# Optimization experiments

Hardware: AMD Instinct MI355X
Metric: run time of the kernel (lower is better)

The kernel has to match this reference:

```python
import jax, jax.numpy as jnp
import numpy as np

B, NORM_NC, LABEL_NC, STYLE_SIZE, NHIDDEN, H, W, KS = 8, 256, 19, 512, 128, 128, 128, 3
EPS = 1e-5


def conv2d(x, w, b):
    # NCHW conv, stride 1, SAME padding (pw = ks//2)
    y = jax.lax.conv_general_dilated(x, w, window_strides=(1, 1), padding='SAME',
                                     dimension_numbers=('NCHW', 'OIHW', 'NCHW'))
    return y + b[None, :, None, None]


def setup_inputs() -> dict:
    key = jax.random.key(0)
    ks = jax.random.split(key, 16)
    s = 0.05
    return {
        'x': jax.random.normal(ks[0], (B, NORM_NC, H, W), jnp.float32),
        'segmap': jax.random.uniform(ks[1], (B, LABEL_NC, H, W), jnp.float32),
        'style': jax.random.normal(ks[2], (B, LABEL_NC, STYLE_SIZE), jnp.float32),
        'w_shared': jax.random.normal(ks[3], (NHIDDEN, LABEL_NC, KS, KS), jnp.float32) * s,
        'b_shared': jnp.zeros((NHIDDEN,), jnp.float32),
        'w_gamma': jax.random.normal(ks[4], (NORM_NC, NHIDDEN, KS, KS), jnp.float32) * s,
        'b_gamma': jnp.zeros((NORM_NC,), jnp.float32),
        'w_beta': jax.random.normal(ks[5], (NORM_NC, NHIDDEN, KS, KS), jnp.float32) * s,
        'b_beta': jnp.zeros((NORM_NC,), jnp.float32),
        'w_sgamma': jax.random.normal(ks[6], (NORM_NC, STYLE_SIZE, KS, KS), jnp.float32) * s,
        'b_sgamma': jnp.zeros((NORM_NC,), jnp.float32),
        'w_sbeta': jax.random.normal(ks[7], (NORM_NC, STYLE_SIZE, KS, KS), jnp.float32) * s,
        'b_sbeta': jnp.zeros((NORM_NC,), jnp.float32),
        'alpha_beta': jax.random.uniform(ks[8], (1,), jnp.float32),
        'alpha_gamma': jax.random.uniform(ks[9], (1,), jnp.float32),
    }


def reference(x, segmap, style, w_shared, b_shared, w_gamma, b_gamma, w_beta, b_beta,
              w_sgamma, b_sgamma, w_sbeta, b_sbeta, alpha_beta, alpha_gamma):
    # InstanceNorm2d (affine=False): per-(b,c) normalization over HxW, biased var
    mean = jnp.mean(x, axis=(2, 3), keepdims=True)
    var = jnp.var(x, axis=(2, 3), keepdims=True)
    normalized = (x - mean) * jax.lax.rsqrt(var + EPS)

    # segmap already at fm_size == out_size -> nearest interpolate is identity
    actv = jax.nn.relu(conv2d(segmap, w_shared, b_shared))  # (B, nhidden, H, W)

    # fused per-pixel contraction over label channels:
    # (style[b,l,s] * segmap[b,l,h,w]).sum(l) -> (B, style_size, H, W)
    style_map = jnp.einsum('bls,blhw->bshw', style, segmap)

    gamma = conv2d(actv, w_gamma, b_gamma)
    beta = conv2d(actv, w_beta, b_beta)
    gamma_style = conv2d(style_map, w_sgamma, b_sgamma)
    beta_style = conv2d(style_map, w_sbeta, b_sbeta)

    wb = jax.nn.sigmoid(alpha_beta)[0]
    wg = jax.nn.sigmoid(alpha_gamma)[0]
    combined_offset = wb * beta_style + (1.0 - wb) * beta
    combined_scale = wg * gamma_style + (1.0 - wg) * gamma + 1.0
    return normalized * combined_scale + combined_offset
```

## Files before the change

### kernel.cpp

```cpp
#include <hip/hip_runtime.h>
#include <hip/hip_bf16.h>
#include <cstdint>

#define B_ 8
#define LABEL_NC 19
#define H_ 128
#define W_ 128
#define UC 640
#define EPS_ 1e-5f

typedef __attribute__((ext_vector_type(8))) short s8v;
typedef __attribute__((ext_vector_type(4))) float f4v;
typedef __attribute__((ext_vector_type(4))) int i4v;
typedef unsigned short ushort_t;

__device__ __forceinline__ ushort_t f2b(float f) {
    union { float f; uint32_t u; } a; a.f = f;
    uint32_t u = a.u;
    return (ushort_t)((u + 0x7FFFu + ((u >> 16) & 1u)) >> 16);
}

__device__ __forceinline__ void gl2lds16(const ushort_t* g, ushort_t* l) {
    __builtin_amdgcn_global_load_lds(
        (const __attribute__((address_space(1))) unsigned int*)g,
        (__attribute__((address_space(3))) unsigned int*)l, 16, 0, 0);
}

__global__ void __launch_bounds__(256) k_prep(
    const float* __restrict__ w_gamma, const float* __restrict__ w_beta,
    const float* __restrict__ w_sgamma, const float* __restrict__ w_sbeta,
    const float* __restrict__ b_gamma, const float* __restrict__ b_beta,
    const float* __restrict__ b_sgamma, const float* __restrict__ b_sbeta,
    const float* __restrict__ alpha_beta, const float* __restrict__ alpha_gamma,
    ushort_t* __restrict__ Wt, float* __restrict__ bias_s, float* __restrict__ bias_o,
    float* __restrict__ zpage)
{
    float wb = 1.f / (1.f + __expf(-alpha_beta[0]));
    float wg = 1.f / (1.f + __expf(-alpha_gamma[0]));
    int gid = blockIdx.x * 256 + threadIdx.x;
    if (gid < 256) bias_s[gid] = wg * b_sgamma[gid] + (1.f - wg) * b_gamma[gid];
    else if (gid < 512) bias_o[gid - 256] = wb * b_sbeta[gid - 256] + (1.f - wb) * b_beta[gid - 256];
    if (gid < 8192) zpage[gid] = 0.f;

    const int total = 9 * 512 * 640;
    for (int idx = gid; idx < total; idx += gridDim.x * 256) {
        int tap = idx / (512 * 640);
        int r = idx - tap * (512 * 640);
        int co = r / 640, ci = r - co * 640;
        int kh = tap / 3, kw = tap - kh * 3;
        float v;
        if (co < 256) {
            if (ci < 128) v = (1.f - wg) * w_gamma[((co * 128 + ci) * 3 + kh) * 3 + kw];
            else          v = wg * w_sgamma[((co * 512 + (ci - 128)) * 3 + kh) * 3 + kw];
        } else {
            int c2 = co - 256;
            if (ci < 128) v = (1.f - wb) * w_beta[((c2 * 128 + ci) * 3 + kh) * 3 + kw];
            else          v = wb * w_sbeta[((c2 * 512 + (ci - 128)) * 3 + kh) * 3 + kw];
        }
        Wt[idx] = f2b(v);
    }
}

__global__ void __launch_bounds__(256) k_stats(const float* __restrict__ x,
                                               float* __restrict__ mean, float* __restrict__ rstd)
{
    int bc = blockIdx.x;
    const float4* p = (const float4*)(x + (size_t)bc * (H_ * W_));
    float s = 0.f, s2 = 0.f;
    for (int i = threadIdx.x; i < H_ * W_ / 4; i += 256) {
        float4 v = p[i];
        s += v.x + v.y + v.z + v.w;
        s2 += v.x * v.x + v.y * v.y + v.z * v.z + v.w * v.w;
    }
    #pragma unroll
    for (int o = 32; o > 0; o >>= 1) { s += __shfl_xor(s, o); s2 += __shfl_xor(s2, o); }
    __shared__ float red[8];
    int wave = threadIdx.x >> 6, lane = threadIdx.x & 63;
    if (lane == 0) { red[wave] = s; red[wave + 4] = s2; }
    __syncthreads();
    if (threadIdx.x == 0) {
        float ts = red[0] + red[1] + red[2] + red[3];
        float t2 = red[4] + red[5] + red[6] + red[7];
        float m = ts * (1.f / 16384.f);
        float v = t2 * (1.f / 16384.f) - m * m;
        mean[bc] = m;
        rstd[bc] = rsqrtf(v + EPS_);
    }
}

__global__ void __launch_bounds__(256) k_buildU(
    const float* __restrict__ segmap, const float* __restrict__ style,
    const float* __restrict__ w_shared, const float* __restrict__ b_shared,
    ushort_t* __restrict__ U)
{
    int bh = blockIdx.x;
    int b = bh >> 7, h = bh & 127;
    __shared__ float seg[3][LABEL_NC][W_];
    const float* segb = segmap + (size_t)b * (LABEL_NC * H_ * W_);
    for (int idx = threadIdx.x; idx < 3 * LABEL_NC * W_; idx += 256) {
        int w = idx & 127;
        int l = (idx >> 7) % LABEL_NC;
        int rr = idx / (LABEL_NC * W_);
        int hh = h + rr - 1;
        seg[rr][l][w] = (hh >= 0 && hh < H_) ? segb[((size_t)l * H_ + hh) * W_ + w] : 0.f;
    }
    __syncthreads();

    int t = threadIdx.x;
    int w = t & 127;
    int grp = __builtin_amdgcn_readfirstlane(t >> 7);
    ushort_t* Urow = U + (((size_t)(b * H_ + h)) * W_ + w) * UC;

    for (int cb = 0; cb < 4; ++cb) {
        int co0 = grp * 64 + cb * 16;
        float acc[16];
        #pragma unroll
        for (int i = 0; i < 16; ++i) acc[i] = b_shared[co0 + i];
        for (int l = 0; l < LABEL_NC; ++l) {
            #pragma unroll
            for (int kh = 0; kh < 3; ++kh) {
                float sm = (w > 0)   ? seg[kh][l][w - 1] : 0.f;
                float s0 = seg[kh][l][w];
                float sp = (w < 127) ? seg[kh][l][w + 1] : 0.f;
                const float* wp = w_shared + ((size_t)co0 * LABEL_NC + l) * 9 + kh * 3;
                #pragma unroll
                for (int i = 0; i < 16; ++i) {
                    const float* wpi = wp + i * (LABEL_NC * 9);
                    acc[i] += sm * wpi[0] + s0 * wpi[1] + sp * wpi[2];
                }
            }
        }
        #pragma unroll
        for (int i = 0; i < 16; ++i)
            Urow[co0 + i] = f2b(acc[i] > 0.f ? acc[i] : 0.f);
    }

    float segr[LABEL_NC];
    #pragma unroll
    for (int l = 0; l < LABEL_NC; ++l) segr[l] = seg[1][l][w];
    const float* styb = style + (size_t)b * (LABEL_NC * 512);
    for (int sb = 0; sb < 16; ++sb) {
        int s0 = grp * 256 + sb * 16;
        float acc[16];
        #pragma unroll
        for (int i = 0; i < 16; ++i) acc[i] = 0.f;
        for (int l = 0; l < LABEL_NC; ++l) {
            const float* sp = styb + l * 512 + s0;
            float sl = segr[l];
            #pragma unroll
            for (int i = 0; i < 16; ++i) acc[i] += sl * sp[i];
        }
        #pragma unroll
        for (int i = 0; i < 16; ++i) Urow[128 + s0 + i] = f2b(acc[i]);
    }
}

#define BK 32

__global__ void __launch_bounds__(512, 1) k_conv(
    const ushort_t* __restrict__ U, const ushort_t* __restrict__ Wt,
    const ushort_t* __restrict__ zp,
    const float* __restrict__ x, const float* __restrict__ mean, const float* __restrict__ rstd,
    const float* __restrict__ bias_s, const float* __restrict__ bias_o,
    float* __restrict__ out)
{
    int orig = blockIdx.x;
    int wg = (orig & 7) * 128 + (orig >> 3);
    int mtile = wg >> 1;
    int cohalf = wg & 1;
    int b = mtile >> 6;
    int h0 = (mtile & 63) << 1;

    extern __shared__ ushort_t smem[];

    int t = threadIdx.x;
    int wv = t >> 6, ln = t & 63;
    int wm = wv >> 1, wn = wv & 1;

    const ushort_t* Ub = U + (size_t)b * (H_ * W_ * UC);

    f4v acc[4][8] = {};

    auto stage_A = [&](int ci0, int ab) {
        ushort_t* sAb = smem + ab * 16384;
        #pragma unroll
        for (int i = 0; i < 4; ++i) {
            int issue = wv * 4 + i;
            int hh = h0 - 1 + (issue >> 3);
            int w = issue * 16 + (ln >> 2);
            int sl = (ln & 3) ^ ((w >> 1) & 3);
            const ushort_t* src = (hh >= 0 && hh < H_)
                ? Ub + ((size_t)hh * W_ + (w & 127)) * UC + ci0 + (sl << 3)
                : zp + (size_t)ln * 8;
            gl2lds16(src, sAb + (size_t)issue * 512);
        }
    };
    auto stage_B = [&](int tapX, int ci0X, int bi) {
        ushort_t* base = smem + 32768 + bi * 8192;
        #pragma unroll
        for (int j = 0; j < 2; ++j) {
            int issue = wv * 2 + j;
            int c = issue * 16 + (ln >> 2);
            int sl = (ln & 3) ^ ((c >> 1) & 3);
            int gq = (c >> 6) & 1;
            int cbase = ((c >> 7) << 6) + (c & 63);
            int co = gq * 256 + cohalf * 128 + cbase;
            const ushort_t* src = Wt + ((size_t)tapX * 512 + co) * UC + ci0X + (sl << 3);
            gl2lds16(src, base + (size_t)issue * 512);
        }
    };

    stage_A(0, 0);
    stage_B(0, 0, 0);
    stage_B(1, 0, 1);

    for (int ch = 0; ch < 20; ++ch) {
        int ci0 = ch * BK;
        ushort_t* sAb = smem + (ch & 1) * 16384;
        bool lastch = (ch == 19);
        #pragma unroll
        for (int tap = 0; tap < 9; ++tap) {
            const int dhp1 = tap / 3;
            const int dw = tap - dhp1 * 3 - 1;
            const int bi = tap % 3;
            const int bi2 = (tap + 2) % 3;

            if (tap == 8) {
                if (lastch) { asm volatile("s_waitcnt vmcnt(0)" ::: "memory"); }
                else        { asm volatile("s_waitcnt vmcnt(6)" ::: "memory"); }
            } else          { asm volatile("s_waitcnt vmcnt(2)" ::: "memory"); }
            __builtin_amdgcn_s_barrier();

            if (tap < 7)        stage_B(tap + 2, ci0, bi2);
            else if (!lastch) {
                if (tap == 7) { stage_B(0, ci0 + BK, bi2); stage_A(ci0 + BK, (ch + 1) & 1); }
                else          stage_B(1, ci0 + BK, bi2);
            }

            ushort_t* sBb = smem + 32768 + bi * 8192;
            int sd = ln >> 4;
            s8v af[4];
            #pragma unroll
            for (int mi = 0; mi < 4; ++mi) {
                int p = wm * 64 + mi * 16 + (ln & 15);
                int q = (p & 127) + dw;
                int qc = q < 0 ? 0 : (q > 127 ? 127 : q);
                int r = (p >> 7) + dhp1;
                s8v v = *(const s8v*)&sAb[(size_t)(((r * 128 + qc) << 2) + (sd ^ ((qc >> 1) & 3))) * 8];
                if (dw != 0 && (q < 0 || q > 127)) { s8v z = {}; v = z; }
                af[mi] = v;
            }
            s8v bf[8];
            #pragma unroll
            for (int ni = 0; ni < 8; ++ni) {
                int c = wn * 128 + (ni >> 2) * 64 + (ni & 3) * 16 + (ln & 15);
                bf[ni] = *(const s8v*)&sBb[(size_t)((c << 2) + (sd ^ ((c >> 1) & 3))) * 8];
            }
            __builtin_amdgcn_s_setprio(1);
            #pragma unroll
            for (int mi = 0; mi < 4; ++mi)
                #pragma unroll
                for (int ni = 0; ni < 8; ++ni)
                    acc[mi][ni] = __builtin_amdgcn_mfma_f32_16x16x32_bf16(
                        af[mi], bf[ni], acc[mi][ni], 0, 0, 0);
            __builtin_amdgcn_s_setprio(0);
        }
    }

    int bc_base = b * 256;
    #pragma unroll
    for (int ni = 0; ni < 4; ++ni) {
        int chn = cohalf * 128 + wn * 64 + ni * 16 + (ln & 15);
        float bs = bias_s[chn] + 1.f;
        float bo = bias_o[chn];
        float mu = mean[bc_base + chn];
        float rs = rstd[bc_base + chn];
        #pragma unroll
        for (int mi = 0; mi < 4; ++mi) {
            #pragma unroll
            for (int r = 0; r < 4; ++r) {
                int p = wm * 64 + mi * 16 + ((ln >> 4) << 2) + r;
                int hh = h0 + (p >> 7);
                int ww = p & 127;
                size_t xi = (((size_t)(bc_base + chn)) * H_ + hh) * W_ + ww;
                float xn = (x[xi] - mu) * rs;
                out[xi] = xn * (acc[mi][ni][r] + bs) + (acc[mi][ni + 4][r] + bo);
            }
        }
    }
}

extern "C" void kernel_launch(void* const* d_in, const int* in_sizes, int n_in,
                              void* d_out, int out_size, void* d_ws, size_t ws_size,
                              hipStream_t stream)
{
    const float* x        = (const float*)d_in[0];
    const float* segmap   = (const float*)d_in[1];
    const float* style    = (const float*)d_in[2];
    const float* w_shared = (const float*)d_in[3];
    const float* b_shared = (const float*)d_in[4];
    const float* w_gamma  = (const float*)d_in[5];
    const float* b_gamma  = (const float*)d_in[6];
    const float* w_beta   = (const float*)d_in[7];
    const float* b_beta   = (const float*)d_in[8];
    const float* w_sgamma = (const float*)d_in[9];
    const float* b_sgamma = (const float*)d_in[10];
    const float* w_sbeta  = (const float*)d_in[11];
    const float* b_sbeta  = (const float*)d_in[12];
    const float* alpha_beta  = (const float*)d_in[13];
    const float* alpha_gamma = (const float*)d_in[14];
    float* out = (float*)d_out;

    char* ws = (char*)d_ws;
    float*    ws_mean  = (float*)(ws + 0);
    float*    ws_rstd  = (float*)(ws + 8192);
    float*    ws_bs    = (float*)(ws + 16384);
    float*    ws_bo    = (float*)(ws + 18432);
    ushort_t* ws_Wt    = (ushort_t*)(ws + 20480);
    ushort_t* ws_zp    = (ushort_t*)(ws + 6 * 1024 * 1024 - 65536);
    ushort_t* ws_U     = (ushort_t*)(ws + 6 * 1024 * 1024);

    (void)hipFuncSetAttribute((const void*)k_conv,
                              hipFuncAttributeMaxDynamicSharedMemorySize, 114688);

    k_prep<<<dim3(2048), dim3(256), 0, stream>>>(w_gamma, w_beta, w_sgamma, w_sbeta,
                                                 b_gamma, b_beta, b_sgamma, b_sbeta,
                                                 alpha_beta, alpha_gamma, ws_Wt, ws_bs, ws_bo,
                                                 (float*)ws_zp);
    k_stats<<<dim3(2048), dim3(256), 0, stream>>>(x, ws_mean, ws_rstd);
    k_buildU<<<dim3(1024), dim3(256), 0, stream>>>(segmap, style, w_shared, b_shared, ws_U);
    k_conv<<<dim3(1024), dim3(512), 114688, stream>>>(ws_U, ws_Wt, ws_zp, x, ws_mean, ws_rstd,
                                                      ws_bs, ws_bo, out);
}
```

Measured before the change: 946.5 us.

## Stage weight tiles in groups of three taps with double-buffered LDS

The conv main loop now loads the B (weight) tiles for a whole kernel row (three taps) at once into one of two LDS buffers. Before, it loaded one tap at a time into a triple-buffered ring. This cuts barriers and waitcnt points from nine to three per input-channel chunk, which amortizes sync overhead over more MFMA work. The cost is more dynamic shared memory (160KB instead of 112KB), longer prefetch bursts, and stricter full vmcnt(0) waits at most group boundaries.

```diff
diff --git a/kernel.cpp b/kernel.cpp
--- a/kernel.cpp
+++ b/kernel.cpp
@@ -195,57 +195,56 @@
             gl2lds16(src, sAb + (size_t)issue * 512);
         }
     };
-    auto stage_B = [&](int tapX, int ci0X, int bi) {
-        ushort_t* base = smem + 32768 + bi * 8192;
-        #pragma unroll
-        for (int j = 0; j < 2; ++j) {
-            int issue = wv * 2 + j;
-            int c = issue * 16 + (ln >> 2);
-            int sl = (ln & 3) ^ ((c >> 1) & 3);
-            int gq = (c >> 6) & 1;
-            int cbase = ((c >> 7) << 6) + (c & 63);
-            int co = gq * 256 + cohalf * 128 + cbase;
-            const ushort_t* src = Wt + ((size_t)tapX * 512 + co) * UC + ci0X + (sl << 3);
-            gl2lds16(src, base + (size_t)issue * 512);
+    auto stage_Bgrp = [&](int dhp1, int ci0X, int bb) {
+        ushort_t* base = smem + 32768 + bb * 24576;
+        #pragma unroll
+        for (int tp = 0; tp < 3; ++tp) {
+            int tapX = dhp1 * 3 + tp;
+            ushort_t* sub = base + tp * 8192;
+            #pragma unroll
+            for (int j = 0; j < 2; ++j) {
+                int issue = wv * 2 + j;
+                int c = issue * 16 + (ln >> 2);
+                int sl = (ln & 3) ^ ((c >> 1) & 3);
+                int gq = (c >> 6) & 1;
+                int cbase = ((c >> 7) << 6) + (c & 63);
+                int co = gq * 256 + cohalf * 128 + cbase;
+                const ushort_t* src = Wt + ((size_t)tapX * 512 + co) * UC + ci0X + (sl << 3);
+                gl2lds16(src, sub + (size_t)issue * 512);
+            }
         }
     };
 
     stage_A(0, 0);
-    stage_B(0, 0, 0);
-    stage_B(1, 0, 1);
-
-    for (int ch = 0; ch < 20; ++ch) {
-        int ci0 = ch * BK;
+    stage_Bgrp(0, 0, 0);
+
+    int ch = 0, gi = 0;
+    for (int g = 0; g < 60; ++g) {
+        if (gi == 2 && ch < 19) { asm volatile("s_waitcnt vmcnt(4)" ::: "memory"); }
+        else                    { asm volatile("s_waitcnt vmcnt(0)" ::: "memory"); }
+        __builtin_amdgcn_s_barrier();
+
+        if (g + 1 < 60) {
+            int chn = (gi == 2) ? ch + 1 : ch;
+            int gin = (gi == 2) ? 0 : gi + 1;
+            stage_Bgrp(gin, chn * BK, (g + 1) & 1);
+        }
+        if (gi == 1 && ch < 19) stage_A((ch + 1) * BK, (ch + 1) & 1);
+
         ushort_t* sAb = smem + (ch & 1) * 16384;
-        bool lastch = (ch == 19);
-        #pragma unroll
-        for (int tap = 0; tap < 9; ++tap) {
-            const int dhp1 = tap / 3;
-            const int dw = tap - dhp1 * 3 - 1;
-            const int bi = tap % 3;
-            const int bi2 = (tap + 2) % 3;
-
-            if (tap == 8) {
-                if (lastch) { asm volatile("s_waitcnt vmcnt(0)" ::: "memory"); }
-                else        { asm volatile("s_waitcnt vmcnt(6)" ::: "memory"); }
-            } else          { asm volatile("s_waitcnt vmcnt(2)" ::: "memory"); }
-            __builtin_amdgcn_s_barrier();
-
-            if (tap < 7)        stage_B(tap + 2, ci0, bi2);
-            else if (!lastch) {
-                if (tap == 7) { stage_B(0, ci0 + BK, bi2); stage_A(ci0 + BK, (ch + 1) & 1); }
-                else          stage_B(1, ci0 + BK, bi2);
-            }
-
-            ushort_t* sBb = smem + 32768 + bi * 8192;
-            int sd = ln >> 4;
+        ushort_t* bbase = smem + 32768 + (g & 1) * 24576;
+        int sd = ln >> 4;
+        #pragma unroll
+        for (int tp = 0; tp < 3; ++tp) {
+            const int dw = tp - 1;
+            ushort_t* sBb = bbase + tp * 8192;
             s8v af[4];
             #pragma unroll
             for (int mi = 0; mi < 4; ++mi) {
                 int p = wm * 64 + mi * 16 + (ln & 15);
                 int q = (p & 127) + dw;
                 int qc = q < 0 ? 0 : (q > 127 ? 127 : q);
-                int r = (p >> 7) + dhp1;
+                int r = (p >> 7) + gi;
                 s8v v = *(const s8v*)&sAb[(size_t)(((r * 128 + qc) << 2) + (sd ^ ((qc >> 1) & 3))) * 8];
                 if (dw != 0 && (q < 0 || q > 127)) { s8v z = {}; v = z; }
                 af[mi] = v;
@@ -264,7 +263,10 @@
                     acc[mi][ni] = __builtin_amdgcn_mfma_f32_16x16x32_bf16(
                         af[mi], bf[ni], acc[mi][ni], 0, 0, 0);
             __builtin_amdgcn_s_setprio(0);
-        }
+            __builtin_amdgcn_sched_barrier(0);
+        }
+
+        if (++gi == 3) { gi = 0; ++ch; }
     }
 
     int bc_base = b * 256;
@@ -321,7 +323,7 @@
     ushort_t* ws_U     = (ushort_t*)(ws + 6 * 1024 * 1024);
 
     (void)hipFuncSetAttribute((const void*)k_conv,
-                              hipFuncAttributeMaxDynamicSharedMemorySize, 114688);
+                              hipFuncAttributeMaxDynamicSharedMemorySize, 163840);
 
     k_prep<<<dim3(2048), dim3(256), 0, stream>>>(w_gamma, w_beta, w_sgamma, w_sbeta,
                                                  b_gamma, b_beta, b_sgamma, b_sbeta,
@@ -329,6 +331,6 @@
                                                  (float*)ws_zp);
     k_stats<<<dim3(2048), dim3(256), 0, stream>>>(x, ws_mean, ws_rstd);
     k_buildU<<<dim3(1024), dim3(256), 0, stream>>>(segmap, style, w_shared, b_shared, ws_U);
-    k_conv<<<dim3(1024), dim3(512), 114688, stream>>>(ws_U, ws_Wt, ws_zp, x, ws_mean, ws_rstd,
+    k_conv<<<dim3(1024), dim3(512), 163840, stream>>>(ws_U, ws_Wt, ws_zp, x, ws_mean, ws_rstd,
                                                       ws_bs, ws_bo, out);
 }
```

New measurement: 969.5 us. +2.4%, slower.

## Double-buffer register fragments to overlap LDS reads with MFMA in conv kernel

Applied to the files above, without the earlier changes.

Restructures the conv main loop so the A/B fragments for the next tap are read from LDS into a second register set while MFMAs run on the current set. Adds a 4-stage B buffer schedule with prefetch distance three, and moves staging of A earlier. The goal is to hide LDS read latency behind matrix work. The cost is extra VGPR pressure from two fragment sets, plus added lgkmcnt waits before each barrier.

```diff
diff --git a/kernel.cpp b/kernel.cpp
--- a/kernel.cpp
+++ b/kernel.cpp
@@ -157,6 +157,32 @@
 
 #define BK 32
 
+#define READ_FRAGS(AF, BF, DHP1, DW, SBB, SAB) { \
+    _Pragma("unroll") \
+    for (int mi = 0; mi < 4; ++mi) { \
+        int p_ = wm * 64 + mi * 16 + (ln & 15); \
+        int q_ = (p_ & 127) + (DW); \
+        int qc_ = q_ < 0 ? 0 : (q_ > 127 ? 127 : q_); \
+        int r_ = (p_ >> 7) + (DHP1); \
+        s8v v_ = *(const s8v*)&(SAB)[(size_t)(((r_ * 128 + qc_) << 2) + (sd ^ ((qc_ >> 1) & 3))) * 8]; \
+        if ((DW) != 0 && (q_ < 0 || q_ > 127)) { s8v z_ = {}; v_ = z_; } \
+        AF[mi] = v_; \
+    } \
+    _Pragma("unroll") \
+    for (int ni = 0; ni < 8; ++ni) { \
+        int c_ = wn * 128 + (ni >> 2) * 64 + (ni & 3) * 16 + (ln & 15); \
+        BF[ni] = *(const s8v*)&(SBB)[(size_t)((c_ << 2) + (sd ^ ((c_ >> 1) & 3))) * 8]; \
+    } }
+
+#define MFMA_SET(AF, BF) { \
+    __builtin_amdgcn_s_setprio(1); \
+    _Pragma("unroll") \
+    for (int mi = 0; mi < 4; ++mi) \
+        _Pragma("unroll") \
+        for (int ni = 0; ni < 8; ++ni) \
+            acc[mi][ni] = __builtin_amdgcn_mfma_f32_16x16x32_bf16(AF[mi], BF[ni], acc[mi][ni], 0, 0, 0); \
+    __builtin_amdgcn_s_setprio(0); }
+
 __global__ void __launch_bounds__(512, 1) k_conv(
     const ushort_t* __restrict__ U, const ushort_t* __restrict__ Wt,
     const ushort_t* __restrict__ zp,
@@ -176,10 +202,12 @@
     int t = threadIdx.x;
     int wv = t >> 6, ln = t & 63;
     int wm = wv >> 1, wn = wv & 1;
+    int sd = ln >> 4;
 
     const ushort_t* Ub = U + (size_t)b * (H_ * W_ * UC);
 
     f4v acc[4][8] = {};
+    s8v afA[4], bfA[8], afB[4], bfB[8];
 
     auto stage_A = [&](int ci0, int ab) {
         ushort_t* sAb = smem + ab * 16384;
@@ -213,57 +241,54 @@
     stage_A(0, 0);
     stage_B(0, 0, 0);
     stage_B(1, 0, 1);
-
-    for (int ch = 0; ch < 20; ++ch) {
-        int ci0 = ch * BK;
-        ushort_t* sAb = smem + (ch & 1) * 16384;
-        bool lastch = (ch == 19);
-        #pragma unroll
-        for (int tap = 0; tap < 9; ++tap) {
-            const int dhp1 = tap / 3;
-            const int dw = tap - dhp1 * 3 - 1;
-            const int bi = tap % 3;
-            const int bi2 = (tap + 2) % 3;
-
-            if (tap == 8) {
-                if (lastch) { asm volatile("s_waitcnt vmcnt(0)" ::: "memory"); }
-                else        { asm volatile("s_waitcnt vmcnt(6)" ::: "memory"); }
-            } else          { asm volatile("s_waitcnt vmcnt(2)" ::: "memory"); }
-            __builtin_amdgcn_s_barrier();
-
-            if (tap < 7)        stage_B(tap + 2, ci0, bi2);
-            else if (!lastch) {
-                if (tap == 7) { stage_B(0, ci0 + BK, bi2); stage_A(ci0 + BK, (ch + 1) & 1); }
-                else          stage_B(1, ci0 + BK, bi2);
+    asm volatile("s_waitcnt vmcnt(2)" ::: "memory");
+    __builtin_amdgcn_s_barrier();
+    READ_FRAGS(afA, bfA, 0, -1, (smem + 32768), smem);
+
+    for (int chp = 0; chp < 10; ++chp) {
+        #pragma unroll
+        for (int half = 0; half < 2; ++half) {
+            int ch = chp * 2 + half;
+            int ci0 = ch * BK;
+            bool lastch = (ch == 19);
+            bool firstch = (ch == 0);
+            ushort_t* sAb = smem + (ch & 1) * 16384;
+            ushort_t* sAn = smem + ((ch + 1) & 1) * 16384;
+            #pragma unroll
+            for (int tap = 0; tap < 9; ++tap) {
+                const int par = (half + tap) & 1;
+
+                if (firstch && tap == 0)     { asm volatile("s_waitcnt vmcnt(0)" ::: "memory"); }
+                else if (lastch && tap >= 7) { asm volatile("s_waitcnt vmcnt(0)" ::: "memory"); }
+                else if (!lastch && (tap == 6 || tap == 7))
+                                             { asm volatile("s_waitcnt vmcnt(6)" ::: "memory"); }
+                else                         { asm volatile("s_waitcnt vmcnt(2)" ::: "memory"); }
+                asm volatile("s_waitcnt lgkmcnt(0)" ::: "memory");
+                __builtin_amdgcn_s_barrier();
+
+                if (firstch && tap == 0) stage_B(2, ci0, 2);
+                if (tap <= 5) {
+                    stage_B(tap + 3, ci0, tap % 3);
+                    if (tap == 5 && !lastch) stage_A(ci0 + BK, (ch + 1) & 1);
+                } else if (!lastch) {
+                    stage_B(tap - 6, ci0 + BK, tap % 3);
+                }
+
+                if (tap < 8) {
+                    const int tp = tap + 1;
+                    const int dh2 = tp / 3, dw2 = tp % 3 - 1;
+                    ushort_t* sBn = smem + 32768 + (tp % 3) * 8192;
+                    if (par == 0) { READ_FRAGS(afB, bfB, dh2, dw2, sBn, sAb) }
+                    else          { READ_FRAGS(afA, bfA, dh2, dw2, sBn, sAb) }
+                } else if (!lastch) {
+                    ushort_t* sBn = smem + 32768;
+                    if (par == 0) { READ_FRAGS(afB, bfB, 0, -1, sBn, sAn) }
+                    else          { READ_FRAGS(afA, bfA, 0, -1, sBn, sAn) }
+                }
+
+                if (par == 0) { MFMA_SET(afA, bfA) }
+                else          { MFMA_SET(afB, bfB) }
             }
-
-            ushort_t* sBb = smem + 32768 + bi * 8192;
-            int sd = ln >> 4;
-            s8v af[4];
-            #pragma unroll
-            for (int mi = 0; mi < 4; ++mi) {
-                int p = wm * 64 + mi * 16 + (ln & 15);
-                int q = (p & 127) + dw;
-                int qc = q < 0 ? 0 : (q > 127 ? 127 : q);
-                int r = (p >> 7) + dhp1;
-                s8v v = *(const s8v*)&sAb[(size_t)(((r * 128 + qc) << 2) + (sd ^ ((qc >> 1) & 3))) * 8];
-                if (dw != 0 && (q < 0 || q > 127)) { s8v z = {}; v = z; }
-                af[mi] = v;
-            }
-            s8v bf[8];
-            #pragma unroll
-            for (int ni = 0; ni < 8; ++ni) {
-                int c = wn * 128 + (ni >> 2) * 64 + (ni & 3) * 16 + (ln & 15);
-                bf[ni] = *(const s8v*)&sBb[(size_t)((c << 2) + (sd ^ ((c >> 1) & 3))) * 8];
-            }
-            __builtin_amdgcn_s_setprio(1);
-            #pragma unroll
-            for (int mi = 0; mi < 4; ++mi)
-                #pragma unroll
-                for (int ni = 0; ni < 8; ++ni)
-                    acc[mi][ni] = __builtin_amdgcn_mfma_f32_16x16x32_bf16(
-                        af[mi], bf[ni], acc[mi][ni], 0, 0, 0);
-            __builtin_amdgcn_s_setprio(0);
         }
     }
 
```

New measurement: 2.530 ms. 167% more time.

## Load conv A operand directly from global memory instead of staging through LDS

Applied to the files above, without the earlier changes.

The activation (A) tile is no longer staged into a double-buffered LDS region. Each wave now loads its A fragments straight from global memory every tap, using precomputed row and column offsets, and zeroes fragments that fall on padding borders. The pixel-to-wave mapping changes so each wave covers one output row, which lets the epilogue use float4 loads and stores of x and out. The zero page and dynamic shared memory are removed, so LDS drops to the B buffers only. In exchange, each tap reloads the same A data from global or cache nine times, and those loads are exposed latency with no prefetch.

```diff
diff --git a/kernel.cpp b/kernel.cpp
--- a/kernel.cpp
+++ b/kernel.cpp
@@ -11,7 +11,6 @@
 
 typedef __attribute__((ext_vector_type(8))) short s8v;
 typedef __attribute__((ext_vector_type(4))) float f4v;
-typedef __attribute__((ext_vector_type(4))) int i4v;
 typedef unsigned short ushort_t;
 
 __device__ __forceinline__ ushort_t f2b(float f) {
@@ -32,15 +31,13 @@
     const float* __restrict__ b_gamma, const float* __restrict__ b_beta,
     const float* __restrict__ b_sgamma, const float* __restrict__ b_sbeta,
     const float* __restrict__ alpha_beta, const float* __restrict__ alpha_gamma,
-    ushort_t* __restrict__ Wt, float* __restrict__ bias_s, float* __restrict__ bias_o,
-    float* __restrict__ zpage)
+    ushort_t* __restrict__ Wt, float* __restrict__ bias_s, float* __restrict__ bias_o)
 {
     float wb = 1.f / (1.f + __expf(-alpha_beta[0]));
     float wg = 1.f / (1.f + __expf(-alpha_gamma[0]));
     int gid = blockIdx.x * 256 + threadIdx.x;
     if (gid < 256) bias_s[gid] = wg * b_sgamma[gid] + (1.f - wg) * b_gamma[gid];
     else if (gid < 512) bias_o[gid - 256] = wb * b_sbeta[gid - 256] + (1.f - wb) * b_beta[gid - 256];
-    if (gid < 8192) zpage[gid] = 0.f;
 
     const int total = 9 * 512 * 640;
     for (int idx = gid; idx < total; idx += gridDim.x * 256) {
@@ -159,7 +156,6 @@
 
 __global__ void __launch_bounds__(512, 1) k_conv(
     const ushort_t* __restrict__ U, const ushort_t* __restrict__ Wt,
-    const ushort_t* __restrict__ zp,
     const float* __restrict__ x, const float* __restrict__ mean, const float* __restrict__ rstd,
     const float* __restrict__ bias_s, const float* __restrict__ bias_o,
     float* __restrict__ out)
@@ -171,32 +167,41 @@
     int b = mtile >> 6;
     int h0 = (mtile & 63) << 1;
 
-    extern __shared__ ushort_t smem[];
+    __shared__ ushort_t sB[3 * 8192];
 
     int t = threadIdx.x;
     int wv = t >> 6, ln = t & 63;
     int wm = wv >> 1, wn = wv & 1;
+    int sd = ln >> 4;
 
     const ushort_t* Ub = U + (size_t)b * (H_ * W_ * UC);
 
+    int pxb = (wm & 1) * 64 + (ln & 15);
+    size_t rowoff[3];
+    #pragma unroll
+    for (int dh = 0; dh < 3; ++dh) {
+        int hh = h0 + (wm >> 1) + dh - 1;
+        int hc = hh < 0 ? 0 : (hh > 127 ? 127 : hh);
+        rowoff[dh] = (size_t)hc * (W_ * UC);
+    }
+    bool zr0 = (h0 + (wm >> 1) - 1) < 0;
+    bool zr2 = (h0 + (wm >> 1) + 1) > 127;
+    int qoff[3][4];
+    #pragma unroll
+    for (int dwi = 0; dwi < 3; ++dwi)
+        #pragma unroll
+        for (int mi = 0; mi < 4; ++mi) {
+            int q = pxb + mi * 16 + dwi - 1;
+            int qc = q < 0 ? 0 : (q > 127 ? 127 : q);
+            qoff[dwi][mi] = qc * UC + sd * 8;
+        }
+    bool zlo = ((wm & 1) == 0) && ((ln & 15) == 0);
+    bool zhi = ((wm & 1) == 1) && ((ln & 15) == 15);
+
     f4v acc[4][8] = {};
 
-    auto stage_A = [&](int ci0, int ab) {
-        ushort_t* sAb = smem + ab * 16384;
-        #pragma unroll
-        for (int i = 0; i < 4; ++i) {
-            int issue = wv * 4 + i;
-            int hh = h0 - 1 + (issue >> 3);
-            int w = issue * 16 + (ln >> 2);
-            int sl = (ln & 3) ^ ((w >> 1) & 3);
-            const ushort_t* src = (hh >= 0 && hh < H_)
-                ? Ub + ((size_t)hh * W_ + (w & 127)) * UC + ci0 + (sl << 3)
-                : zp + (size_t)ln * 8;
-            gl2lds16(src, sAb + (size_t)issue * 512);
-        }
-    };
     auto stage_B = [&](int tapX, int ci0X, int bi) {
-        ushort_t* base = smem + 32768 + bi * 8192;
+        ushort_t* base = sB + bi * 8192;
         #pragma unroll
         for (int j = 0; j < 2; ++j) {
             int issue = wv * 2 + j;
@@ -210,64 +215,60 @@
         }
     };
 
-    stage_A(0, 0);
     stage_B(0, 0, 0);
     stage_B(1, 0, 1);
 
     for (int ch = 0; ch < 20; ++ch) {
         int ci0 = ch * BK;
-        ushort_t* sAb = smem + (ch & 1) * 16384;
-        bool lastch = (ch == 19);
         #pragma unroll
         for (int tap = 0; tap < 9; ++tap) {
             const int dhp1 = tap / 3;
-            const int dw = tap - dhp1 * 3 - 1;
+            const int dwi = tap % 3;
             const int bi = tap % 3;
-            const int bi2 = (tap + 2) % 3;
-
-            if (tap == 8) {
-                if (lastch) { asm volatile("s_waitcnt vmcnt(0)" ::: "memory"); }
-                else        { asm volatile("s_waitcnt vmcnt(6)" ::: "memory"); }
-            } else          { asm volatile("s_waitcnt vmcnt(2)" ::: "memory"); }
+
+            if (tap == 8 && ch == 19) { asm volatile("s_waitcnt vmcnt(0)" ::: "memory"); }
+            else                      { asm volatile("s_waitcnt vmcnt(2)" ::: "memory"); }
             __builtin_amdgcn_s_barrier();
 
-            if (tap < 7)        stage_B(tap + 2, ci0, bi2);
-            else if (!lastch) {
-                if (tap == 7) { stage_B(0, ci0 + BK, bi2); stage_A(ci0 + BK, (ch + 1) & 1); }
-                else          stage_B(1, ci0 + BK, bi2);
+            const ushort_t* arow = Ub + rowoff[dhp1] + ci0;
+            s8v av[4];
+            #pragma unroll
+            for (int mi = 0; mi < 4; ++mi)
+                av[mi] = *(const s8v*)(arow + qoff[dwi][mi]);
+
+            {
+                const int tap2 = (tap + 2) % 9;
+                int ch2 = ch + (tap + 2) / 9;
+                if (ch2 < 20) stage_B(tap2, ch2 * BK, (tap + 2) % 3);
             }
 
-            ushort_t* sBb = smem + 32768 + bi * 8192;
-            int sd = ln >> 4;
-            s8v af[4];
-            #pragma unroll
-            for (int mi = 0; mi < 4; ++mi) {
-                int p = wm * 64 + mi * 16 + (ln & 15);
-                int q = (p & 127) + dw;
-                int qc = q < 0 ? 0 : (q > 127 ? 127 : q);
-                int r = (p >> 7) + dhp1;
-                s8v v = *(const s8v*)&sAb[(size_t)(((r * 128 + qc) << 2) + (sd ^ ((qc >> 1) & 3))) * 8];
-                if (dw != 0 && (q < 0 || q > 127)) { s8v z = {}; v = z; }
-                af[mi] = v;
-            }
+            s8v z = {};
+            if (dhp1 == 0) { if (zr0) { av[0] = z; av[1] = z; av[2] = z; av[3] = z; } }
+            if (dhp1 == 2) { if (zr2) { av[0] = z; av[1] = z; av[2] = z; av[3] = z; } }
+            if (dwi == 0) { if (zlo) av[0] = z; }
+            if (dwi == 2) { if (zhi) av[3] = z; }
+
+            ushort_t* sBb = sB + bi * 8192;
             s8v bf[8];
             #pragma unroll
             for (int ni = 0; ni < 8; ++ni) {
                 int c = wn * 128 + (ni >> 2) * 64 + (ni & 3) * 16 + (ln & 15);
                 bf[ni] = *(const s8v*)&sBb[(size_t)((c << 2) + (sd ^ ((c >> 1) & 3))) * 8];
             }
+
             __builtin_amdgcn_s_setprio(1);
             #pragma unroll
             for (int mi = 0; mi < 4; ++mi)
                 #pragma unroll
                 for (int ni = 0; ni < 8; ++ni)
                     acc[mi][ni] = __builtin_amdgcn_mfma_f32_16x16x32_bf16(
-                        af[mi], bf[ni], acc[mi][ni], 0, 0, 0);
+                        av[mi], bf[ni], acc[mi][ni], 0, 0, 0);
             __builtin_amdgcn_s_setprio(0);
         }
     }
 
     int bc_base = b * 256;
+    int hh = h0 + (wm >> 1);
     #pragma unroll
     for (int ni = 0; ni < 4; ++ni) {
         int chn = cohalf * 128 + wn * 64 + ni * 16 + (ln & 15);
@@ -277,15 +278,15 @@
         float rs = rstd[bc_base + chn];
         #pragma unroll
         for (int mi = 0; mi < 4; ++mi) {
-            #pragma unroll
-            for (int r = 0; r < 4; ++r) {
-                int p = wm * 64 + mi * 16 + ((ln >> 4) << 2) + r;
-                int hh = h0 + (p >> 7);
-                int ww = p & 127;
-                size_t xi = (((size_t)(bc_base + chn)) * H_ + hh) * W_ + ww;
-                float xn = (x[xi] - mu) * rs;
-                out[xi] = xn * (acc[mi][ni][r] + bs) + (acc[mi][ni + 4][r] + bo);
-            }
+            int p = (wm & 1) * 64 + mi * 16 + ((ln >> 4) << 2);
+            size_t xi = (((size_t)(bc_base + chn)) * H_ + hh) * W_ + p;
+            float4 xv = *(const float4*)&x[xi];
+            float4 ov;
+            ov.x = (xv.x - mu) * rs * (acc[mi][ni][0] + bs) + (acc[mi][ni + 4][0] + bo);
+            ov.y = (xv.y - mu) * rs * (acc[mi][ni][1] + bs) + (acc[mi][ni + 4][1] + bo);
+            ov.z = (xv.z - mu) * rs * (acc[mi][ni][2] + bs) + (acc[mi][ni + 4][2] + bo);
+            ov.w = (xv.w - mu) * rs * (acc[mi][ni][3] + bs) + (acc[mi][ni + 4][3] + bo);
+            *(float4*)&out[xi] = ov;
         }
     }
 }
@@ -317,18 +318,13 @@
     float*    ws_bs    = (float*)(ws + 16384);
     float*    ws_bo    = (float*)(ws + 18432);
     ushort_t* ws_Wt    = (ushort_t*)(ws + 20480);
-    ushort_t* ws_zp    = (ushort_t*)(ws + 6 * 1024 * 1024 - 65536);
     ushort_t* ws_U     = (ushort_t*)(ws + 6 * 1024 * 1024);
-
-    (void)hipFuncSetAttribute((const void*)k_conv,
-                              hipFuncAttributeMaxDynamicSharedMemorySize, 114688);
 
     k_prep<<<dim3(2048), dim3(256), 0, stream>>>(w_gamma, w_beta, w_sgamma, w_sbeta,
                                                  b_gamma, b_beta, b_sgamma, b_sbeta,
-                                                 alpha_beta, alpha_gamma, ws_Wt, ws_bs, ws_bo,
-                                                 (float*)ws_zp);
+                                                 alpha_beta, alpha_gamma, ws_Wt, ws_bs, ws_bo);
     k_stats<<<dim3(2048), dim3(256), 0, stream>>>(x, ws_mean, ws_rstd);
     k_buildU<<<dim3(1024), dim3(256), 0, stream>>>(segmap, style, w_shared, b_shared, ws_U);
-    k_conv<<<dim3(1024), dim3(512), 114688, stream>>>(ws_U, ws_Wt, ws_zp, x, ws_mean, ws_rstd,
-                                                      ws_bs, ws_bo, out);
-}
+    k_conv<<<dim3(1024), dim3(512), 0, stream>>>(ws_U, ws_Wt, x, ws_mean, ws_rstd,
+                                                 ws_bs, ws_bo, out);
+}
```

Measured after the change: 1.976 ms. 2.09x slower.
